# Kernel tuning notes

Hardware: AMD Instinct MI355X
Metric: run time of the kernel (lower is better)

Reference implementation:

```python
import jax, jax.numpy as jnp
import numpy as np

TEMPERATURE = 0.07
IGNORE_INDEX = -100
NEG_INF = -1e30


def setup_inputs() -> dict:
    key = jax.random.key(0)
    kg, ke, kl = jax.random.split(key, 3)
    B, P, H = 4, 4096, 256
    greek_embeds = jax.random.normal(kg, (B, P, H), dtype=jnp.float32)
    english_embeds = jax.random.normal(ke, (B, P, H), dtype=jnp.float32)
    # labels in {1 aligned, 0 not aligned, -100 ignore}, ~1/3 each
    raw = jax.random.randint(kl, (B, P), 0, 3)
    labels = jnp.where(raw == 2, IGNORE_INDEX, raw).astype(jnp.int32)
    return {"greek_embeds": greek_embeds, "english_embeds": english_embeds, "labels": labels}


def reference(greek_embeds, english_embeds, labels):
    # L2-normalize (F.normalize semantics: clamp norm at 1e-12)
    g = greek_embeds / jnp.clip(jnp.linalg.norm(greek_embeds, axis=-1, keepdims=True), 1e-12)
    e = english_embeds / jnp.clip(jnp.linalg.norm(english_embeds, axis=-1, keepdims=True), 1e-12)
    # [B, P, P] similarity
    sim = jnp.einsum("bph,bqh->bpq", g, e) / TEMPERATURE

    valid = labels != IGNORE_INDEX            # [B, P]
    pos = valid & (labels == 1)               # [B, P]
    neg = valid & (labels != 1)               # [B, P]
    # batch is processed only if >=2 valid pairs AND at least one pos AND one neg
    batch_ok = (valid.sum(-1) >= 2) & pos.any(-1) & neg.any(-1)  # [B]

    diag = jnp.diagonal(sim, axis1=1, axis2=2)                   # [B, P] positive logit
    neg_sims = jnp.where(neg[:, None, :], sim, NEG_INF)          # [B, P, P] negative logits
    # stable logsumexp over concat([diag_i], neg_sims_i)
    m = jnp.maximum(diag, neg_sims.max(-1))                      # [B, P]
    lse = m + jnp.log(jnp.exp(diag - m) + jnp.sum(jnp.exp(neg_sims - m[..., None]), -1))
    per_pos_loss = lse - diag                                    # cross_entropy with target=0

    mask = pos & batch_ok[:, None]
    count = mask.sum()
    total = jnp.sum(jnp.where(mask, per_pos_loss, 0.0))
    return jnp.where(count == 0, 0.0, total / count.astype(total.dtype))
```

## Files before the change

kernel.cpp:

```cpp
#include <hip/hip_runtime.h>
#include <hip/hip_bf16.h>
#include <math.h>

#define BB 4
#define PP 4096
#define HH 256
#define INV_T (1.0f/0.07f)
#define NRB 64
#define TPC 32
#define NTILES (PP/16)
#define TILE_BYTES 8192
#define D2GRID (NRB*32)

typedef __attribute__((ext_vector_type(8))) short bf16x8;
typedef __attribute__((ext_vector_type(4))) float f32x4;

#define WAITVM(n) asm volatile("s_waitcnt vmcnt(" #n ")" ::: "memory")

__device__ __forceinline__ unsigned short f2bf(float x){
  union { float f; unsigned u; } v; v.f = x;
  unsigned r = v.u + 0x7FFFu + ((v.u >> 16) & 1u);
  return (unsigned short)(r >> 16);
}

__device__ __forceinline__ void gload_lds16(const void* g, void* l){
  __builtin_amdgcn_global_load_lds(
      (const __attribute__((address_space(1))) unsigned int*)g,
      (__attribute__((address_space(3))) unsigned int*)l, 16, 0, 0);
}

__global__ void k_prep(const float* __restrict__ greek, const float* __restrict__ english,
                       const int* __restrict__ labels,
                       unsigned short* __restrict__ Gn, unsigned short* __restrict__ EnF,
                       float* __restrict__ diagN, int* __restrict__ posIdx,
                       int* __restrict__ meta, unsigned* __restrict__ negBits){
  int tid = threadIdx.x, wave = tid >> 6, lane = tid & 63;
  if (blockIdx.x < BB){
    int b = blockIdx.x;
    const int* lab = labels + b * PP;
    __shared__ int wP[4], wN[4], wV[4];
    __shared__ int basePos, baseNeg, baseVal;
    if (tid == 0){ basePos = 0; baseNeg = 0; baseVal = 0; }
    __syncthreads();
    for (int c = 0; c < PP; c += 256){
      int p = c + tid;
      int l = lab[p];
      bool isP = (l == 1), isN = (l == 0), isV = (l != -100);
      unsigned long long bP = __ballot(isP), bN = __ballot(isN), bV = __ballot(isV);
      unsigned long long lt = (1ull << lane) - 1ull;
      if (lane == 0){
        wP[wave] = __popcll(bP); wN[wave] = __popcll(bN); wV[wave] = __popcll(bV);
        int w0 = (c + (wave << 6)) >> 5;
        negBits[b*128 + w0]     = (unsigned)bN;
        negBits[b*128 + w0 + 1] = (unsigned)(bN >> 32);
      }
      __syncthreads();
      int offP = 0;
      for (int w = 0; w < wave; w++) offP += wP[w];
      if (isP) posIdx[b*PP + basePos + offP + __popcll(bP & lt)] = p;
      __syncthreads();
      if (tid == 0){
        basePos += wP[0]+wP[1]+wP[2]+wP[3];
        baseNeg += wN[0]+wN[1]+wN[2]+wN[3];
        baseVal += wV[0]+wV[1]+wV[2]+wV[3];
      }
      __syncthreads();
    }
    if (tid == 0){
      int Np = basePos, Nn = baseNeg, nv = baseVal;
      meta[b*4+0] = Np; meta[b*4+1] = Nn;
      meta[b*4+2] = (nv >= 2 && Np > 0 && Nn > 0) ? 1 : 0;
      meta[b*4+3] = nv;
    }
  } else {
    int u = (blockIdx.x - BB) * 4 + wave;
    int lab = labels[u];
    if (lab == -100) return;
    int b = u >> 12, i = u & (PP-1);
    size_t base = (size_t)u * HH + lane * 4;
    if (lab == 1){
      float4 g4 = *reinterpret_cast<const float4*>(greek + base);
      float4 e4 = *reinterpret_cast<const float4*>(english + base);
      float ag = g4.x*g4.x + g4.y*g4.y + g4.z*g4.z + g4.w*g4.w;
      float ae = e4.x*e4.x + e4.y*e4.y + e4.z*e4.z + e4.w*e4.w;
      float ad = g4.x*e4.x + g4.y*e4.y + g4.z*e4.z + g4.w*e4.w;
      #pragma unroll
      for (int off = 32; off; off >>= 1){
        ag += __shfl_xor(ag, off); ae += __shfl_xor(ae, off); ad += __shfl_xor(ad, off);
      }
      float gs = 1.0f / fmaxf(sqrtf(ag), 1e-12f);
      float es = 1.0f / fmaxf(sqrtf(ae), 1e-12f);
      ushort4 go; go.x=f2bf(g4.x*gs); go.y=f2bf(g4.y*gs); go.z=f2bf(g4.z*gs); go.w=f2bf(g4.w*gs);
      *reinterpret_cast<ushort4*>(Gn + (size_t)u*HH + lane*4) = go;
      if (lane == 0) diagN[u] = ad * gs * es;
    } else {
      float4 e4 = *reinterpret_cast<const float4*>(english + base);
      float ae = e4.x*e4.x + e4.y*e4.y + e4.z*e4.z + e4.w*e4.w;
      #pragma unroll
      for (int off = 32; off; off >>= 1) ae += __shfl_xor(ae, off);
      float es = 1.0f / fmaxf(sqrtf(ae), 1e-12f);
      unsigned u0 = (unsigned)f2bf(e4.x*es) | ((unsigned)f2bf(e4.y*es) << 16);
      unsigned u1 = (unsigned)f2bf(e4.z*es) | ((unsigned)f2bf(e4.w*es) << 16);
      unsigned o0 = __shfl_xor(u0, 1), o1 = __shfl_xor(u1, 1);
      char* dst = (char*)EnF + ((size_t)b*NTILES + (i>>4))*TILE_BYTES
                + (lane>>3)*1024 + (((i&15) + ((lane>>1)&3)*16) << 4);
      if (!(lane & 1)) *(uint4*)dst = make_uint4(u0, u1, o0, o1);
    }
  }
}

__global__ void __launch_bounds__(256, 4)
k_loss(const unsigned short* __restrict__ Gn, const unsigned short* __restrict__ EnF,
       const int* __restrict__ posIdx, const int* __restrict__ meta,
       const unsigned* __restrict__ negBits, float* __restrict__ Spart){
  int L = blockIdx.x;
  int rb = L >> 5, b = (L >> 3) & 3, chunk = L & 7;
  int tid = threadIdx.x, wave = tid >> 6, lane = tid & 63;
  int lo16 = lane & 15, hi4 = lane >> 4;
  int Np = meta[b*4+0], ok = meta[b*4+2];
  int i0 = rb * 64;
  if (!ok || i0 >= Np) return;

  __shared__ __align__(16) char Bs[3][TILE_BYTES];

  unsigned mymask = 0;
  const unsigned* nbp = negBits + b*128 + chunk*16;
  #pragma unroll
  for (int w = 0; w < 16; w++){
    unsigned word = nbp[w];
    mymask |= ((word >> lo16) & 1u) << (2*w);
    mymask |= ((word >> (lo16 + 16)) & 1u) << (2*w + 1);
  }

  int iw = i0 + wave*16;
  int ii = min(iw + lo16, Np-1);
  int prow = posIdx[b*PP + ii];
  const char* Ab = (const char*)Gn + ((size_t)b*PP + prow)*(HH*2) + hi4*16;
  bf16x8 a[8];
  #pragma unroll
  for (int kk = 0; kk < 8; kk++)
    a[kk] = *reinterpret_cast<const bf16x8*>(Ab + kk*64);

  const char* EFb = (const char*)EnF + (size_t)b * NTILES * TILE_BYTES;
  int T0 = chunk * TPC;

  auto STAGE = [&](int t, int buf){
    const char* src = EFb + (size_t)t*TILE_BYTES + (wave << 11) + (lane << 4);
    char* d = &Bs[buf][wave << 11];
    gload_lds16(src, d);
    gload_lds16(src + 1024, d + 1024);
  };
  STAGE(T0, 0);
  STAGE(T0+1, 1);

  float s[4] = {0.f,0.f,0.f,0.f};
  int cur = 0;
  for (int t = T0; t < T0 + TPC; t++){
    if (t + 1 < T0 + TPC) WAITVM(2);
    else                  WAITVM(0);
    __builtin_amdgcn_s_barrier();
    __builtin_amdgcn_sched_barrier(0);
    if (t + 2 < T0 + TPC){
      int nbuf = cur + 2; if (nbuf >= 3) nbuf -= 3;
      STAGE(t+2, nbuf);
    }
    const char* Bt = &Bs[cur][0];
    f32x4 c = {0.f,0.f,0.f,0.f};
    #pragma unroll
    for (int kk = 0; kk < 8; kk++){
      bf16x8 bv = *reinterpret_cast<const bf16x8*>(Bt + kk*1024 + (lane << 4));
      c = __builtin_amdgcn_mfma_f32_16x16x32_bf16(a[kk], bv, c, 0, 0, 0);
    }
    bool cok = (mymask >> (t - T0)) & 1;
    #pragma unroll
    for (int r = 0; r < 4; r++)
      s[r] += cok ? __expf(c[r] * INV_T) : 0.0f;
    cur = (cur == 2) ? 0 : cur + 1;
  }

  #pragma unroll
  for (int off = 1; off < 16; off <<= 1){
    #pragma unroll
    for (int r = 0; r < 4; r++) s[r] += __shfl_xor(s[r], off);
  }
  if (lo16 == 0){
    #pragma unroll
    for (int r = 0; r < 4; r++){
      int i = iw + hi4*4 + r;
      Spart[(((size_t)b*PP + i) << 3) + chunk] = s[r];
    }
  }
}

__global__ void k_final(const float* __restrict__ Spart, const float* __restrict__ diagN,
                        const int* __restrict__ posIdx, const int* __restrict__ meta,
                        float* __restrict__ out){
  __shared__ float lds[16];
  int tid = threadIdx.x;
  int np[BB], okk[BB];
  #pragma unroll
  for (int b = 0; b < BB; b++){ np[b] = meta[b*4+0]; okk[b] = meta[b*4+2]; }
  float tot = 0.0f;
  for (int idx = tid; idx < BB*PP; idx += 1024){
    int b = idx >> 12, i = idx & (PP-1);
    if (!okk[b] || i >= np[b]) continue;
    const float4* p = reinterpret_cast<const float4*>(Spart + ((size_t)idx << 3));
    float4 p0 = p[0], p1 = p[1];
    float S = ((p0.x+p0.y)+(p0.z+p0.w)) + ((p1.x+p1.y)+(p1.z+p1.w));
    float dl = diagN[b*PP + posIdx[idx]] * INV_T;
    tot += logf(S + __expf(dl)) - dl;
  }
  #pragma unroll
  for (int off = 32; off; off >>= 1) tot += __shfl_xor(tot, off);
  int wave = tid >> 6;
  if ((tid & 63) == 0) lds[wave] = tot;
  __syncthreads();
  if (tid == 0){
    float total = 0.0f;
    #pragma unroll
    for (int w = 0; w < 16; w++) total += lds[w];
    int count = 0;
    #pragma unroll
    for (int b = 0; b < BB; b++) if (okk[b]) count += np[b];
    out[0] = (count == 0) ? 0.0f : total / (float)count;
  }
}

extern "C" void kernel_launch(void* const* d_in, const int* in_sizes, int n_in,
                              void* d_out, int out_size, void* d_ws, size_t ws_size,
                              hipStream_t stream){
  const float* greek   = (const float*)d_in[0];
  const float* english = (const float*)d_in[1];
  const int*   labels  = (const int*)d_in[2];
  float* out = (float*)d_out;

  char* ws = (char*)d_ws;
  size_t off = 0;
  unsigned short* Gn   = (unsigned short*)(ws + off); off += (size_t)BB*PP*HH*2;
  unsigned short* EnF  = (unsigned short*)(ws + off); off += (size_t)BB*NTILES*TILE_BYTES;
  float* Spart      = (float*)(ws + off); off += (size_t)BB*PP*8*sizeof(float);
  float* diagN      = (float*)(ws + off); off += (size_t)BB*PP*sizeof(float);
  int*   posIdx     = (int*)(ws + off);   off += (size_t)BB*PP*sizeof(int);
  int*   meta       = (int*)(ws + off);   off += 64;
  unsigned* negBits = (unsigned*)(ws + off); off += (size_t)BB*128*sizeof(unsigned);

  k_prep<<<BB + BB*PP/4, 256, 0, stream>>>(greek, english, labels, Gn, EnF, diagN,
                                           posIdx, meta, negBits);
  k_loss<<<D2GRID, 256, 0, stream>>>(Gn, EnF, posIdx, meta, negBits, Spart);
  k_final<<<1, 1024, 0, stream>>>(Spart, diagN, posIdx, meta, out);
}
```

Measured before the change: 45.25 us.

## Compact negative columns and process two row tiles per wave in loss kernel

The label scan is split into its own kernel, which computes a compacted rank for each negative column. Normalized English rows are then written densely by that rank, so the loss kernel walks only ceil(Nn/16) tiles and skips the non-negative columns (about two thirds of them). Each wave now holds two 16-row A fragments and shares every LDS B-tile read across two MFMA chains. Row blocks double to 128 rows, which halves the active grid. The cost is one extra kernel launch, a serialized scan before normalization, and higher register pressure.

```diff
diff --git a/kernel.cpp b/kernel.cpp
--- a/kernel.cpp
+++ b/kernel.cpp
@@ -6,10 +6,11 @@
 #define PP 4096
 #define HH 256
 #define INV_T (1.0f/0.07f)
-#define NRB 64
-#define TPC 32
+#define JSPLIT 8
 #define NTILES (PP/16)
 #define TILE_BYTES 8192
+#define RBROWS 128
+#define NRB (PP/RBROWS)
 #define D2GRID (NRB*32)
 
 typedef __attribute__((ext_vector_type(8))) short bf16x8;
@@ -29,165 +30,170 @@
       (__attribute__((address_space(3))) unsigned int*)l, 16, 0, 0);
 }
 
-__global__ void k_prep(const float* __restrict__ greek, const float* __restrict__ english,
-                       const int* __restrict__ labels,
+__global__ void k_scan(const int* __restrict__ labels, int* __restrict__ meta,
+                       int* __restrict__ posIdx, int* __restrict__ negRank){
+  int b = blockIdx.x;
+  const int* lab = labels + b * PP;
+  __shared__ int wP[4], wN[4], wV[4];
+  __shared__ int basePos, baseNeg, baseVal;
+  int tid = threadIdx.x, wave = tid >> 6, lane = tid & 63;
+  if (tid == 0){ basePos = 0; baseNeg = 0; baseVal = 0; }
+  __syncthreads();
+  for (int c = 0; c < PP; c += 256){
+    int p = c + tid;
+    int l = lab[p];
+    bool isP = (l == 1), isN = (l == 0), isV = (l != -100);
+    unsigned long long bP = __ballot(isP), bN = __ballot(isN), bV = __ballot(isV);
+    unsigned long long lt = (1ull << lane) - 1ull;
+    if (lane == 0){ wP[wave] = __popcll(bP); wN[wave] = __popcll(bN); wV[wave] = __popcll(bV); }
+    __syncthreads();
+    int offP = 0, offN = 0;
+    for (int w = 0; w < wave; w++){ offP += wP[w]; offN += wN[w]; }
+    if (isP) posIdx[b*PP + basePos + offP + __popcll(bP & lt)] = p;
+    if (isN) negRank[b*PP + p] = baseNeg + offN + __popcll(bN & lt);
+    __syncthreads();
+    if (tid == 0){
+      basePos += wP[0]+wP[1]+wP[2]+wP[3];
+      baseNeg += wN[0]+wN[1]+wN[2]+wN[3];
+      baseVal += wV[0]+wV[1]+wV[2]+wV[3];
+    }
+    __syncthreads();
+  }
+  if (tid == 0){
+    int Np = basePos, Nn = baseNeg, nv = baseVal;
+    meta[b*4+0] = Np; meta[b*4+1] = Nn;
+    meta[b*4+2] = (nv >= 2 && Np > 0 && Nn > 0) ? 1 : 0;
+    meta[b*4+3] = nv;
+  }
+}
+
+__global__ void k_norm(const float* __restrict__ greek, const float* __restrict__ english,
+                       const int* __restrict__ labels, const int* __restrict__ negRank,
                        unsigned short* __restrict__ Gn, unsigned short* __restrict__ EnF,
-                       float* __restrict__ diagN, int* __restrict__ posIdx,
-                       int* __restrict__ meta, unsigned* __restrict__ negBits){
+                       float* __restrict__ diagN){
   int tid = threadIdx.x, wave = tid >> 6, lane = tid & 63;
-  if (blockIdx.x < BB){
-    int b = blockIdx.x;
-    const int* lab = labels + b * PP;
-    __shared__ int wP[4], wN[4], wV[4];
-    __shared__ int basePos, baseNeg, baseVal;
-    if (tid == 0){ basePos = 0; baseNeg = 0; baseVal = 0; }
-    __syncthreads();
-    for (int c = 0; c < PP; c += 256){
-      int p = c + tid;
-      int l = lab[p];
-      bool isP = (l == 1), isN = (l == 0), isV = (l != -100);
-      unsigned long long bP = __ballot(isP), bN = __ballot(isN), bV = __ballot(isV);
-      unsigned long long lt = (1ull << lane) - 1ull;
-      if (lane == 0){
-        wP[wave] = __popcll(bP); wN[wave] = __popcll(bN); wV[wave] = __popcll(bV);
-        int w0 = (c + (wave << 6)) >> 5;
-        negBits[b*128 + w0]     = (unsigned)bN;
-        negBits[b*128 + w0 + 1] = (unsigned)(bN >> 32);
-      }
-      __syncthreads();
-      int offP = 0;
-      for (int w = 0; w < wave; w++) offP += wP[w];
-      if (isP) posIdx[b*PP + basePos + offP + __popcll(bP & lt)] = p;
-      __syncthreads();
-      if (tid == 0){
-        basePos += wP[0]+wP[1]+wP[2]+wP[3];
-        baseNeg += wN[0]+wN[1]+wN[2]+wN[3];
-        baseVal += wV[0]+wV[1]+wV[2]+wV[3];
-      }
-      __syncthreads();
-    }
-    if (tid == 0){
-      int Np = basePos, Nn = baseNeg, nv = baseVal;
-      meta[b*4+0] = Np; meta[b*4+1] = Nn;
-      meta[b*4+2] = (nv >= 2 && Np > 0 && Nn > 0) ? 1 : 0;
-      meta[b*4+3] = nv;
-    }
+  int u = blockIdx.x * 4 + wave;
+  int lab = labels[u];
+  if (lab == -100) return;
+  int b = u >> 12;
+  size_t base = (size_t)u * HH + lane * 4;
+  if (lab == 1){
+    float4 g4 = *reinterpret_cast<const float4*>(greek + base);
+    float4 e4 = *reinterpret_cast<const float4*>(english + base);
+    float ag = g4.x*g4.x + g4.y*g4.y + g4.z*g4.z + g4.w*g4.w;
+    float ae = e4.x*e4.x + e4.y*e4.y + e4.z*e4.z + e4.w*e4.w;
+    float ad = g4.x*e4.x + g4.y*e4.y + g4.z*e4.z + g4.w*e4.w;
+    #pragma unroll
+    for (int off = 32; off; off >>= 1){
+      ag += __shfl_xor(ag, off); ae += __shfl_xor(ae, off); ad += __shfl_xor(ad, off);
+    }
+    float gs = 1.0f / fmaxf(sqrtf(ag), 1e-12f);
+    float es = 1.0f / fmaxf(sqrtf(ae), 1e-12f);
+    ushort4 go; go.x=f2bf(g4.x*gs); go.y=f2bf(g4.y*gs); go.z=f2bf(g4.z*gs); go.w=f2bf(g4.w*gs);
+    *reinterpret_cast<ushort4*>(Gn + (size_t)u*HH + lane*4) = go;
+    if (lane == 0) diagN[u] = ad * gs * es;
   } else {
-    int u = (blockIdx.x - BB) * 4 + wave;
-    int lab = labels[u];
-    if (lab == -100) return;
-    int b = u >> 12, i = u & (PP-1);
-    size_t base = (size_t)u * HH + lane * 4;
-    if (lab == 1){
-      float4 g4 = *reinterpret_cast<const float4*>(greek + base);
-      float4 e4 = *reinterpret_cast<const float4*>(english + base);
-      float ag = g4.x*g4.x + g4.y*g4.y + g4.z*g4.z + g4.w*g4.w;
-      float ae = e4.x*e4.x + e4.y*e4.y + e4.z*e4.z + e4.w*e4.w;
-      float ad = g4.x*e4.x + g4.y*e4.y + g4.z*e4.z + g4.w*e4.w;
-      #pragma unroll
-      for (int off = 32; off; off >>= 1){
-        ag += __shfl_xor(ag, off); ae += __shfl_xor(ae, off); ad += __shfl_xor(ad, off);
-      }
-      float gs = 1.0f / fmaxf(sqrtf(ag), 1e-12f);
-      float es = 1.0f / fmaxf(sqrtf(ae), 1e-12f);
-      ushort4 go; go.x=f2bf(g4.x*gs); go.y=f2bf(g4.y*gs); go.z=f2bf(g4.z*gs); go.w=f2bf(g4.w*gs);
-      *reinterpret_cast<ushort4*>(Gn + (size_t)u*HH + lane*4) = go;
-      if (lane == 0) diagN[u] = ad * gs * es;
-    } else {
-      float4 e4 = *reinterpret_cast<const float4*>(english + base);
-      float ae = e4.x*e4.x + e4.y*e4.y + e4.z*e4.z + e4.w*e4.w;
-      #pragma unroll
-      for (int off = 32; off; off >>= 1) ae += __shfl_xor(ae, off);
-      float es = 1.0f / fmaxf(sqrtf(ae), 1e-12f);
-      unsigned u0 = (unsigned)f2bf(e4.x*es) | ((unsigned)f2bf(e4.y*es) << 16);
-      unsigned u1 = (unsigned)f2bf(e4.z*es) | ((unsigned)f2bf(e4.w*es) << 16);
-      unsigned o0 = __shfl_xor(u0, 1), o1 = __shfl_xor(u1, 1);
-      char* dst = (char*)EnF + ((size_t)b*NTILES + (i>>4))*TILE_BYTES
-                + (lane>>3)*1024 + (((i&15) + ((lane>>1)&3)*16) << 4);
-      if (!(lane & 1)) *(uint4*)dst = make_uint4(u0, u1, o0, o1);
-    }
+    float4 e4 = *reinterpret_cast<const float4*>(english + base);
+    float ae = e4.x*e4.x + e4.y*e4.y + e4.z*e4.z + e4.w*e4.w;
+    #pragma unroll
+    for (int off = 32; off; off >>= 1) ae += __shfl_xor(ae, off);
+    float es = 1.0f / fmaxf(sqrtf(ae), 1e-12f);
+    unsigned u0 = (unsigned)f2bf(e4.x*es) | ((unsigned)f2bf(e4.y*es) << 16);
+    unsigned u1 = (unsigned)f2bf(e4.z*es) | ((unsigned)f2bf(e4.w*es) << 16);
+    unsigned o0 = __shfl_xor(u0, 1), o1 = __shfl_xor(u1, 1);
+    int rank = negRank[u];
+    char* dst = (char*)EnF + ((size_t)b*NTILES + (rank>>4))*TILE_BYTES
+              + (lane>>3)*1024 + (((rank&15) + ((lane>>1)&3)*16) << 4);
+    if (!(lane & 1)) *(uint4*)dst = make_uint4(u0, u1, o0, o1);
   }
 }
 
 __global__ void __launch_bounds__(256, 4)
 k_loss(const unsigned short* __restrict__ Gn, const unsigned short* __restrict__ EnF,
        const int* __restrict__ posIdx, const int* __restrict__ meta,
-       const unsigned* __restrict__ negBits, float* __restrict__ Spart){
+       float* __restrict__ Spart){
   int L = blockIdx.x;
   int rb = L >> 5, b = (L >> 3) & 3, chunk = L & 7;
   int tid = threadIdx.x, wave = tid >> 6, lane = tid & 63;
   int lo16 = lane & 15, hi4 = lane >> 4;
-  int Np = meta[b*4+0], ok = meta[b*4+2];
-  int i0 = rb * 64;
+  int Np = meta[b*4+0], Nn = meta[b*4+1], ok = meta[b*4+2];
+  int i0 = rb * RBROWS;
   if (!ok || i0 >= Np) return;
 
+  int NT = (Nn + 15) >> 4;
+  int TPC = (NT + JSPLIT - 1) / JSPLIT;
+  int t0 = chunk * TPC, t1 = min(NT, t0 + TPC);
+
   __shared__ __align__(16) char Bs[3][TILE_BYTES];
 
-  unsigned mymask = 0;
-  const unsigned* nbp = negBits + b*128 + chunk*16;
-  #pragma unroll
-  for (int w = 0; w < 16; w++){
-    unsigned word = nbp[w];
-    mymask |= ((word >> lo16) & 1u) << (2*w);
-    mymask |= ((word >> (lo16 + 16)) & 1u) << (2*w + 1);
-  }
-
-  int iw = i0 + wave*16;
-  int ii = min(iw + lo16, Np-1);
-  int prow = posIdx[b*PP + ii];
-  const char* Ab = (const char*)Gn + ((size_t)b*PP + prow)*(HH*2) + hi4*16;
-  bf16x8 a[8];
-  #pragma unroll
-  for (int kk = 0; kk < 8; kk++)
-    a[kk] = *reinterpret_cast<const bf16x8*>(Ab + kk*64);
+  int iw0 = i0 + wave*16;
+  int iw1 = iw0 + 64;
+  int pr0 = posIdx[b*PP + min(iw0 + lo16, Np-1)];
+  int pr1 = posIdx[b*PP + min(iw1 + lo16, Np-1)];
+  const char* Ab0 = (const char*)Gn + ((size_t)b*PP + pr0)*(HH*2) + hi4*16;
+  const char* Ab1 = (const char*)Gn + ((size_t)b*PP + pr1)*(HH*2) + hi4*16;
+  bf16x8 a0[8], a1[8];
+  #pragma unroll
+  for (int kk = 0; kk < 8; kk++){
+    a0[kk] = *reinterpret_cast<const bf16x8*>(Ab0 + kk*64);
+    a1[kk] = *reinterpret_cast<const bf16x8*>(Ab1 + kk*64);
+  }
 
   const char* EFb = (const char*)EnF + (size_t)b * NTILES * TILE_BYTES;
-  int T0 = chunk * TPC;
-
   auto STAGE = [&](int t, int buf){
     const char* src = EFb + (size_t)t*TILE_BYTES + (wave << 11) + (lane << 4);
     char* d = &Bs[buf][wave << 11];
     gload_lds16(src, d);
     gload_lds16(src + 1024, d + 1024);
   };
-  STAGE(T0, 0);
-  STAGE(T0+1, 1);
-
-  float s[4] = {0.f,0.f,0.f,0.f};
-  int cur = 0;
-  for (int t = T0; t < T0 + TPC; t++){
-    if (t + 1 < T0 + TPC) WAITVM(2);
-    else                  WAITVM(0);
-    __builtin_amdgcn_s_barrier();
-    __builtin_amdgcn_sched_barrier(0);
-    if (t + 2 < T0 + TPC){
-      int nbuf = cur + 2; if (nbuf >= 3) nbuf -= 3;
-      STAGE(t+2, nbuf);
-    }
-    const char* Bt = &Bs[cur][0];
-    f32x4 c = {0.f,0.f,0.f,0.f};
-    #pragma unroll
-    for (int kk = 0; kk < 8; kk++){
-      bf16x8 bv = *reinterpret_cast<const bf16x8*>(Bt + kk*1024 + (lane << 4));
-      c = __builtin_amdgcn_mfma_f32_16x16x32_bf16(a[kk], bv, c, 0, 0, 0);
-    }
-    bool cok = (mymask >> (t - T0)) & 1;
-    #pragma unroll
-    for (int r = 0; r < 4; r++)
-      s[r] += cok ? __expf(c[r] * INV_T) : 0.0f;
-    cur = (cur == 2) ? 0 : cur + 1;
+
+  float s0[4] = {0.f,0.f,0.f,0.f}, s1[4] = {0.f,0.f,0.f,0.f};
+  if (t0 < t1){
+    STAGE(t0, 0);
+    if (t0 + 1 < t1) STAGE(t0+1, 1);
+    int cur = 0;
+    for (int t = t0; t < t1; t++){
+      if (t + 1 < t1) WAITVM(2);
+      else            WAITVM(0);
+      __builtin_amdgcn_s_barrier();
+      __builtin_amdgcn_sched_barrier(0);
+      if (t + 2 < t1){
+        int nbuf = cur + 2; if (nbuf >= 3) nbuf -= 3;
+        STAGE(t+2, nbuf);
+      }
+      const char* Bt = &Bs[cur][0];
+      f32x4 c0 = {0.f,0.f,0.f,0.f}, c1 = {0.f,0.f,0.f,0.f};
+      #pragma unroll
+      for (int kk = 0; kk < 8; kk++){
+        bf16x8 bv = *reinterpret_cast<const bf16x8*>(Bt + kk*1024 + (lane << 4));
+        c0 = __builtin_amdgcn_mfma_f32_16x16x32_bf16(a0[kk], bv, c0, 0, 0, 0);
+        c1 = __builtin_amdgcn_mfma_f32_16x16x32_bf16(a1[kk], bv, c1, 0, 0, 0);
+      }
+      bool cok = (t*16 + lo16) < Nn;
+      #pragma unroll
+      for (int r = 0; r < 4; r++){
+        s0[r] += cok ? __expf(c0[r] * INV_T) : 0.0f;
+        s1[r] += cok ? __expf(c1[r] * INV_T) : 0.0f;
+      }
+      cur = (cur == 2) ? 0 : cur + 1;
+    }
   }
 
   #pragma unroll
   for (int off = 1; off < 16; off <<= 1){
     #pragma unroll
-    for (int r = 0; r < 4; r++) s[r] += __shfl_xor(s[r], off);
+    for (int r = 0; r < 4; r++){
+      s0[r] += __shfl_xor(s0[r], off);
+      s1[r] += __shfl_xor(s1[r], off);
+    }
   }
   if (lo16 == 0){
     #pragma unroll
     for (int r = 0; r < 4; r++){
-      int i = iw + hi4*4 + r;
-      Spart[(((size_t)b*PP + i) << 3) + chunk] = s[r];
+      int ia = iw0 + hi4*4 + r;
+      int ib2 = iw1 + hi4*4 + r;
+      Spart[(((size_t)b*PP + ia) << 3) + chunk] = s0[r];
+      Spart[(((size_t)b*PP + ib2) << 3) + chunk] = s1[r];
     }
   }
 }
@@ -241,11 +247,11 @@
   float* Spart      = (float*)(ws + off); off += (size_t)BB*PP*8*sizeof(float);
   float* diagN      = (float*)(ws + off); off += (size_t)BB*PP*sizeof(float);
   int*   posIdx     = (int*)(ws + off);   off += (size_t)BB*PP*sizeof(int);
+  int*   negRank    = (int*)(ws + off);   off += (size_t)BB*PP*sizeof(int);
   int*   meta       = (int*)(ws + off);   off += 64;
-  unsigned* negBits = (unsigned*)(ws + off); off += (size_t)BB*128*sizeof(unsigned);
-
-  k_prep<<<BB + BB*PP/4, 256, 0, stream>>>(greek, english, labels, Gn, EnF, diagN,
-                                           posIdx, meta, negBits);
-  k_loss<<<D2GRID, 256, 0, stream>>>(Gn, EnF, posIdx, meta, negBits, Spart);
+
+  k_scan<<<BB, 256, 0, stream>>>(labels, meta, posIdx, negRank);
+  k_norm<<<BB*PP/4, 256, 0, stream>>>(greek, english, labels, negRank, Gn, EnF, diagN);
+  k_loss<<<D2GRID, 256, 0, stream>>>(Gn, EnF, posIdx, meta, Spart);
   k_final<<<1, 1024, 0, stream>>>(Spart, diagN, posIdx, meta, out);
 }
```

Result: no change. 46.11 us (+1.9%).
